# Optimization experiments

Hardware: AMD Instinct MI355X
Metric: run time of the kernel (lower is better)

Reference implementation:

```python
import jax, jax.numpy as jnp
import numpy as np

B, N, C = 2, 4096, 768
H = 12
D = C // H  # head_dim = 64
SCALE = D ** -0.5


def setup_inputs() -> dict:
    key = jax.random.key(0)
    ks = jax.random.split(key, 5)
    std = C ** -0.5
    return {
        "x": jax.random.normal(ks[0], (B, N, C), dtype=jnp.float32),
        "qkv_w": jax.random.normal(ks[1], (3 * C, C), dtype=jnp.float32) * std,
        "qkv_b": jnp.zeros((3 * C,), dtype=jnp.float32),
        "proj_w": jax.random.normal(ks[2], (C, C), dtype=jnp.float32) * std,
        "proj_b": jnp.zeros((C,), dtype=jnp.float32),
    }


def reference(x, qkv_w, qkv_b, proj_w, proj_b):
    b, n, c = x.shape
    # qkv projection: [B,N,3C] -> [3,B,H,N,D]
    qkv = (x @ qkv_w.T + qkv_b).reshape(b, n, 3, H, D).transpose(2, 0, 3, 1, 4)
    q, k, v = qkv[0], qkv[1], qkv[2]
    # scaled dot-product attention, explicit softmax (fused_attn=False path)
    attn = jnp.einsum("bhqd,bhkd->bhqk", q * SCALE, k)
    attn = jax.nn.softmax(attn, axis=-1)
    out = jnp.einsum("bhqk,bhkd->bhqd", attn, v)
    out = out.transpose(0, 2, 1, 3).reshape(b, n, c)
    return out @ proj_w.T + proj_b
```

## Files before the change

kernel.cpp:

```cpp
#include <hip/hip_runtime.h>
#include <hip/hip_bf16.h>
#include <stdint.h>

#define DEV __device__ __forceinline__

typedef __bf16 bf16_t;
typedef bf16_t bf16x8 __attribute__((ext_vector_type(8)));
typedef float f32x4 __attribute__((ext_vector_type(4)));
typedef unsigned long long ull;

union Frag { bf16x8 v; ull h[2]; };

struct __align__(16) Pack16 { ull lo, hi; };

DEV unsigned short f2b(float f) {
  bf16_t b = (bf16_t)f;
  return __builtin_bit_cast(unsigned short, b);
}

DEV void async_copy16(void* lds, const void* gsrc) {
  __builtin_amdgcn_global_load_lds(
      (const __attribute__((address_space(1))) unsigned int*)(uintptr_t)gsrc,
      (__attribute__((address_space(3))) unsigned int*)(uintptr_t)lds,
      16, 0, 0);
}

#define MFMA16x16x32(a, b, c) __builtin_amdgcn_mfma_f32_16x16x32_bf16((a), (b), (c), 0, 0, 0)

#define QSCALE 0.18033688011112042f

__global__ __launch_bounds__(256) void k_cvt_all(
    const float* __restrict__ s0, Pack16* __restrict__ d0, int n0,
    const float* __restrict__ s1, Pack16* __restrict__ d1, int n1,
    const float* __restrict__ s2, Pack16* __restrict__ d2, int n2) {
  int i = blockIdx.x * 256 + threadIdx.x;
  const float* src; Pack16* dst; int idx;
  if (i < n0) { src = s0; dst = d0; idx = i; }
  else if (i < n0 + n1) { src = s1; dst = d1; idx = i - n0; }
  else if (i < n0 + n1 + n2) { src = s2; dst = d2; idx = i - n0 - n1; }
  else return;
  const float4* s4 = (const float4*)src + 2 * (size_t)idx;
  float4 a = s4[0], b = s4[1];
  union { unsigned short u[8]; Pack16 p; } P;
  P.u[0] = f2b(a.x); P.u[1] = f2b(a.y); P.u[2] = f2b(a.z); P.u[3] = f2b(a.w);
  P.u[4] = f2b(b.x); P.u[5] = f2b(b.y); P.u[6] = f2b(b.z); P.u[7] = f2b(b.w);
  dst[idx] = P.p;
}

template <int EPI>
__global__ __launch_bounds__(256) void k_gemm(
    const unsigned short* __restrict__ A, const unsigned short* __restrict__ Bw,
    const float* __restrict__ bias,
    unsigned short* __restrict__ qp, unsigned short* __restrict__ kp,
    unsigned short* __restrict__ vtp, float* __restrict__ outp,
    int Nn, int K, int nt_n) {
  __shared__ char LDS[2 * 32768];
  const int tid = threadIdx.x;
  const int lane = tid & 63, wid = tid >> 6;
  const int g = lane >> 4, lq = lane & 15;
  const int tm = blockIdx.x / nt_n, tn = blockIdx.x % nt_n;
  const int m0 = tm * 128, n0 = tn * 128;
  const int wm = (wid >> 1) * 64, wn = (wid & 1) * 64;
  const size_t rowbytes = (size_t)K * 2;
  const int nk = K >> 6;
  f32x4 acc[4][4] = {};

  const char* aga[4];
  const char* bga[4];
#pragma unroll
  for (int pass = 0; pass < 4; ++pass) {
    int c = pass * 256 + tid;
    int r = c >> 3;
    int cb = ((c & 7) * 16) ^ ((r & 7) << 4);
    aga[pass] = (const char*)A + (size_t)(m0 + r) * rowbytes + cb;
    bga[pass] = (const char*)Bw + (size_t)(n0 + r) * rowbytes + cb;
  }

#pragma unroll
  for (int pass = 0; pass < 4; ++pass) {
    async_copy16(LDS + pass * 4096 + tid * 16, aga[pass]);
    async_copy16(LDS + 16384 + pass * 4096 + tid * 16, bga[pass]);
    aga[pass] += 128; bga[pass] += 128;
  }
  asm volatile("s_waitcnt vmcnt(0)" ::: "memory");
  __syncthreads();

  int buf = 0;
  for (int ks = 0; ks < nk; ++ks) {
    if (ks < nk - 1) {
      char* nb = LDS + (buf ^ 1) * 32768;
#pragma unroll
      for (int pass = 0; pass < 4; ++pass) {
        async_copy16(nb + pass * 4096 + tid * 16, aga[pass]);
        async_copy16(nb + 16384 + pass * 4096 + tid * 16, bga[pass]);
        aga[pass] += 128; bga[pass] += 128;
      }
    }
    const char* Ab = LDS + buf * 32768;
    const char* Bb = Ab + 16384;
#pragma unroll
    for (int kk = 0; kk < 2; ++kk) {
      Frag aF[4], bF[4];
#pragma unroll
      for (int f = 0; f < 4; ++f) {
        int ra = wm + f * 16 + lq;
        aF[f].v = *(const bf16x8*)(Ab + ra * 128 +
                                   ((kk * 64 + 16 * g) ^ ((ra & 7) << 4)));
        int rb = wn + f * 16 + lq;
        bF[f].v = *(const bf16x8*)(Bb + rb * 128 +
                                   ((kk * 64 + 16 * g) ^ ((rb & 7) << 4)));
      }
#pragma unroll
      for (int fm = 0; fm < 4; ++fm)
#pragma unroll
        for (int fn = 0; fn < 4; ++fn)
          acc[fm][fn] = MFMA16x16x32(aF[fm].v, bF[fn].v, acc[fm][fn]);
    }
    asm volatile("s_waitcnt vmcnt(0)" ::: "memory");
    __syncthreads();
    buf ^= 1;
  }

  if (EPI == 0) {
    const int which = tm / 6;
    const float sc = (which == 0) ? QSCALE : 1.0f;
#pragma unroll
    for (int fm = 0; fm < 4; ++fm) {
#pragma unroll
      for (int fn = 0; fn < 4; ++fn) {
        int f = m0 + wm + fm * 16 + 4 * g;
        int t = n0 + wn + fn * 16 + lq;
        int rem = f - which * 768;
        int hh = rem >> 6, ddb = rem & 63;
        int bb = t >> 12, tr = t & 4095;
        int bh = bb * 12 + hh;
        float4 bq = *(const float4*)(bias + f);
        float bvr[4] = {bq.x, bq.y, bq.z, bq.w};
        if (which == 2) {
#pragma unroll
          for (int r = 0; r < 4; ++r) {
            int d = ddb + r;
            size_t off = (size_t)bh * 262144 + (size_t)(tr >> 6) * 4096 +
                         (size_t)((d >> 4) * 2 + ((tr >> 5) & 1)) * 512 +
                         (size_t)(((tr >> 2) & 3) * 16 + (d & 15)) * 8 +
                         (size_t)((tr >> 4) & 1) * 4 + (size_t)(tr & 3);
            vtp[off] = f2b(acc[fm][fn][r] + bvr[r]);
          }
        } else {
          unsigned short* dst = (which == 0) ? qp : kp;
          union { unsigned short u[4]; ull q; } pk;
#pragma unroll
          for (int r = 0; r < 4; ++r) pk.u[r] = f2b((acc[fm][fn][r] + bvr[r]) * sc);
          *(ull*)(dst + ((size_t)bh * 4096 + tr) * 64 + ddb) = pk.q;
        }
      }
    }
  } else {
#pragma unroll
    for (int fm = 0; fm < 4; ++fm)
#pragma unroll
      for (int fn = 0; fn < 4; ++fn) {
        int f = m0 + wm + fm * 16 + 4 * g;
        int t = n0 + wn + fn * 16 + lq;
        float4 bq = *(const float4*)(bias + f);
        float4 o4;
        o4.x = acc[fm][fn][0] + bq.x;
        o4.y = acc[fm][fn][1] + bq.y;
        o4.z = acc[fm][fn][2] + bq.z;
        o4.w = acc[fm][fn][3] + bq.w;
        *(float4*)(outp + (size_t)t * Nn + f) = o4;
      }
  }
}

__global__ __launch_bounds__(256) void k_attn(
    const unsigned short* __restrict__ qp, const unsigned short* __restrict__ kp,
    const unsigned short* __restrict__ vtp, unsigned short* __restrict__ ao) {
  __shared__ unsigned short KsA[2 * 4096];
  __shared__ unsigned short VsA[2 * 4096];
  const int tid = threadIdx.x;
  const int lane = tid & 63, wid = tid >> 6;
  const int g = lane >> 4, lq = lane & 15;
  const int bh = blockIdx.x % 24, qb = blockIdx.x / 24;
  const int q0 = qb * 128 + wid * 16;
  const unsigned short* qbase = qp + ((size_t)bh * 4096 + q0) * 64;

  Frag qF[2][2];
#pragma unroll
  for (int grp = 0; grp < 2; ++grp)
#pragma unroll
    for (int kk = 0; kk < 2; ++kk)
      qF[grp][kk].v = *(const bf16x8*)(qbase + grp * 4096 + lq * 64 + kk * 32 + 8 * g);

  const char* kga0; const char* kga1;
  const char* vga0; const char* vga1;
  {
    int c = tid;
    int krow = (c >> 7) * 16 + (c & 15);
    int kbyte = ((c >> 6) & 1) * 64 + ((c >> 4) & 3) * 16;
    kga0 = (const char*)(kp + (size_t)bh * 262144) + (size_t)krow * 128 + kbyte;
    kga1 = kga0 + 4096;
    vga0 = (const char*)(vtp + (size_t)bh * 262144) + (size_t)c * 16;
    vga1 = vga0 + 4096;
  }
  char* ldsK = (char*)KsA + tid * 16;
  char* ldsV = (char*)VsA + tid * 16;

  Frag oneF;
#pragma unroll
  for (int j = 0; j < 8; ++j) oneF.v[j] = (bf16_t)1.0f;

  f32x4 o[2][4] = {};
  f32x4 l_acc[2] = {};

  async_copy16(ldsK, kga0);
  async_copy16(ldsK + 4096, kga1);
  async_copy16(ldsV, vga0);
  async_copy16(ldsV + 4096, vga1);
  kga0 += 8192; kga1 += 8192; vga0 += 8192; vga1 += 8192;
  asm volatile("s_waitcnt vmcnt(0)" ::: "memory");
  __syncthreads();

  int cur = 0;
  for (int t = 0; t < 64; ++t) {
    if (t < 63) {
      int nb = (cur ^ 1) * 8192;
      async_copy16(ldsK + nb, kga0);
      async_copy16(ldsK + nb + 4096, kga1);
      async_copy16(ldsV + nb, vga0);
      async_copy16(ldsV + nb + 4096, vga1);
      kga0 += 8192; kga1 += 8192; vga0 += 8192; vga1 += 8192;
    }
    const char* Kb = (const char*)KsA + cur * 8192 + lane * 16;
    const char* Vb = (const char*)VsA + cur * 8192 + lane * 16;

    f32x4 s0[4], s1[4];
    __builtin_amdgcn_s_setprio(1);
#pragma unroll
    for (int fn = 0; fn < 4; ++fn) {
      Frag k0F, k1F;
      k0F.v = *(const bf16x8*)(Kb + (fn * 2 + 0) * 1024);
      k1F.v = *(const bf16x8*)(Kb + (fn * 2 + 1) * 1024);
      f32x4 a0 = {0.f, 0.f, 0.f, 0.f}, a1 = {0.f, 0.f, 0.f, 0.f};
      a0 = MFMA16x16x32(k0F.v, qF[0][0].v, a0);
      a0 = MFMA16x16x32(k1F.v, qF[0][1].v, a0);
      a1 = MFMA16x16x32(k0F.v, qF[1][0].v, a1);
      a1 = MFMA16x16x32(k1F.v, qF[1][1].v, a1);
      s0[fn] = a0; s1[fn] = a1;
    }
    __builtin_amdgcn_s_setprio(0);

    Frag pA0[2], pA1[2];
#pragma unroll
    for (int kk = 0; kk < 2; ++kk)
#pragma unroll
      for (int j = 0; j < 4; ++j) {
        pA0[kk].v[j]     = (bf16_t)__builtin_amdgcn_exp2f(s0[2 * kk][j]);
        pA0[kk].v[4 + j] = (bf16_t)__builtin_amdgcn_exp2f(s0[2 * kk + 1][j]);
        pA1[kk].v[j]     = (bf16_t)__builtin_amdgcn_exp2f(s1[2 * kk][j]);
        pA1[kk].v[4 + j] = (bf16_t)__builtin_amdgcn_exp2f(s1[2 * kk + 1][j]);
      }

    __builtin_amdgcn_s_setprio(1);
    l_acc[0] = MFMA16x16x32(oneF.v, pA0[0].v, l_acc[0]);
    l_acc[0] = MFMA16x16x32(oneF.v, pA0[1].v, l_acc[0]);
    l_acc[1] = MFMA16x16x32(oneF.v, pA1[0].v, l_acc[1]);
    l_acc[1] = MFMA16x16x32(oneF.v, pA1[1].v, l_acc[1]);
#pragma unroll
    for (int d = 0; d < 4; ++d) {
      Frag v0F, v1F;
      v0F.v = *(const bf16x8*)(Vb + (d * 2 + 0) * 1024);
      v1F.v = *(const bf16x8*)(Vb + (d * 2 + 1) * 1024);
      o[0][d] = MFMA16x16x32(v0F.v, pA0[0].v, o[0][d]);
      o[0][d] = MFMA16x16x32(v1F.v, pA0[1].v, o[0][d]);
      o[1][d] = MFMA16x16x32(v0F.v, pA1[0].v, o[1][d]);
      o[1][d] = MFMA16x16x32(v1F.v, pA1[1].v, o[1][d]);
    }
    __builtin_amdgcn_s_setprio(0);

    asm volatile("s_waitcnt vmcnt(0)" ::: "memory");
    __syncthreads();
    cur ^= 1;
  }

  const int bb = bh / 12, hh = bh % 12;
#pragma unroll
  for (int grp = 0; grp < 2; ++grp) {
    float rl = __builtin_amdgcn_rcpf(l_acc[grp][0]);
    int q = q0 + grp * 64 + lq;
    unsigned short* dst = ao + ((size_t)(bb * 4096 + q)) * 768 + hh * 64;
#pragma unroll
    for (int d = 0; d < 4; ++d) {
      union { unsigned short u[4]; ull qw; } pk;
#pragma unroll
      for (int r = 0; r < 4; ++r) pk.u[r] = f2b(o[grp][d][r] * rl);
      *(ull*)(dst + d * 16 + 4 * g) = pk.qw;
    }
  }
}

extern "C" void kernel_launch(void* const* d_in, const int* in_sizes, int n_in,
                              void* d_out, int out_size, void* d_ws, size_t ws_size,
                              hipStream_t stream) {
  (void)in_sizes; (void)n_in; (void)out_size; (void)ws_size;
  const float* x = (const float*)d_in[0];
  const float* qkv_w = (const float*)d_in[1];
  const float* qkv_b = (const float*)d_in[2];
  const float* proj_w = (const float*)d_in[3];
  const float* proj_b = (const float*)d_in[4];
  float* out = (float*)d_out;
  unsigned short* ws = (unsigned short*)d_ws;

  unsigned short* xb    = ws;
  unsigned short* wqkv  = ws + 6291456;
  unsigned short* wproj = ws + 8060928;
  unsigned short* qp    = ws + 8650752;
  unsigned short* kp    = ws + 14942208;
  unsigned short* vtp   = ws + 21233664;
  unsigned short* ao    = xb;

  k_cvt_all<<<4224, 256, 0, stream>>>(x, (Pack16*)xb, 786432,
                                      qkv_w, (Pack16*)wqkv, 221184,
                                      proj_w, (Pack16*)wproj, 73728);

  k_gemm<0><<<18 * 64, 256, 0, stream>>>(wqkv, xb, qkv_b, qp, kp, vtp, nullptr,
                                         2304, 768, 64);
  k_attn<<<768, 256, 0, stream>>>(qp, kp, vtp, ao);
  k_gemm<1><<<6 * 64, 256, 0, stream>>>(wproj, ao, proj_b, nullptr, nullptr, nullptr,
                                        out, 768, 768, 64);
}
```

Baseline: 269.3 us.

## Prefetch two tiles ahead with partial vmcnt waits in GEMM and attention loops

Both the GEMM and the attention kernels now issue async global-to-LDS loads two stages ahead instead of one. Each iteration waits only for the older stage (partial vmcnt), reads the whole tile from LDS into registers, then barriers and refills that same buffer while the MFMAs run. This removes the full vmcnt(0) drain and end-of-iteration syncthreads that serialized memory and compute. The cost is more live registers for the preloaded fragments, which may lower occupancy, and an extra barrier per iteration.

Measured after the change: 291.9 us. +8.4%, slower.

```diff
diff --git a/kernel.cpp b/kernel.cpp
--- a/kernel.cpp
+++ b/kernel.cpp
@@ -76,49 +76,54 @@
     bga[pass] = (const char*)Bw + (size_t)(n0 + r) * rowbytes + cb;
   }
 
-#pragma unroll
-  for (int pass = 0; pass < 4; ++pass) {
-    async_copy16(LDS + pass * 4096 + tid * 16, aga[pass]);
-    async_copy16(LDS + 16384 + pass * 4096 + tid * 16, bga[pass]);
-    aga[pass] += 128; bga[pass] += 128;
-  }
-  asm volatile("s_waitcnt vmcnt(0)" ::: "memory");
-  __syncthreads();
-
-  int buf = 0;
+  auto stageAB = [&](int bufoff) {
+#pragma unroll
+    for (int pass = 0; pass < 4; ++pass) {
+      async_copy16(LDS + bufoff + pass * 4096 + tid * 16, aga[pass]);
+      async_copy16(LDS + bufoff + 16384 + pass * 4096 + tid * 16, bga[pass]);
+      aga[pass] += 128; bga[pass] += 128;
+    }
+  };
+
+  stageAB(0);
+  stageAB(32768);
+
   for (int ks = 0; ks < nk; ++ks) {
-    if (ks < nk - 1) {
-      char* nb = LDS + (buf ^ 1) * 32768;
-#pragma unroll
-      for (int pass = 0; pass < 4; ++pass) {
-        async_copy16(nb + pass * 4096 + tid * 16, aga[pass]);
-        async_copy16(nb + 16384 + pass * 4096 + tid * 16, bga[pass]);
-        aga[pass] += 128; bga[pass] += 128;
-      }
-    }
-    const char* Ab = LDS + buf * 32768;
+    if (ks < nk - 1)
+      asm volatile("s_waitcnt vmcnt(8)" ::: "memory");
+    else
+      asm volatile("s_waitcnt vmcnt(0)" ::: "memory");
+    __builtin_amdgcn_s_barrier();
+
+    const char* Ab = LDS + (ks & 1) * 32768;
     const char* Bb = Ab + 16384;
-#pragma unroll
-    for (int kk = 0; kk < 2; ++kk) {
-      Frag aF[4], bF[4];
+    Frag aF[2][4], bF[2][4];
+#pragma unroll
+    for (int kk = 0; kk < 2; ++kk)
 #pragma unroll
       for (int f = 0; f < 4; ++f) {
         int ra = wm + f * 16 + lq;
-        aF[f].v = *(const bf16x8*)(Ab + ra * 128 +
-                                   ((kk * 64 + 16 * g) ^ ((ra & 7) << 4)));
+        aF[kk][f].v = *(const bf16x8*)(Ab + ra * 128 +
+                                       ((kk * 64 + 16 * g) ^ ((ra & 7) << 4)));
         int rb = wn + f * 16 + lq;
-        bF[f].v = *(const bf16x8*)(Bb + rb * 128 +
-                                   ((kk * 64 + 16 * g) ^ ((rb & 7) << 4)));
+        bF[kk][f].v = *(const bf16x8*)(Bb + rb * 128 +
+                                       ((kk * 64 + 16 * g) ^ ((rb & 7) << 4)));
       }
+    asm volatile("s_waitcnt lgkmcnt(0)" ::: "memory");
+    __builtin_amdgcn_sched_barrier(0);
+    __builtin_amdgcn_s_barrier();
+
+    if (ks + 2 < nk) stageAB((ks & 1) * 32768);
+
+    __builtin_amdgcn_s_setprio(1);
+#pragma unroll
+    for (int kk = 0; kk < 2; ++kk)
 #pragma unroll
       for (int fm = 0; fm < 4; ++fm)
 #pragma unroll
         for (int fn = 0; fn < 4; ++fn)
-          acc[fm][fn] = MFMA16x16x32(aF[fm].v, bF[fn].v, acc[fm][fn]);
-    }
-    asm volatile("s_waitcnt vmcnt(0)" ::: "memory");
-    __syncthreads();
-    buf ^= 1;
+          acc[fm][fn] = MFMA16x16x32(aF[kk][fm].v, bF[kk][fn].v, acc[fm][fn]);
+    __builtin_amdgcn_s_setprio(0);
   }
 
   if (EPI == 0) {
@@ -206,6 +211,14 @@
   char* ldsK = (char*)KsA + tid * 16;
   char* ldsV = (char*)VsA + tid * 16;
 
+  auto stageKV = [&](int bufoff) {
+    async_copy16(ldsK + bufoff, kga0);
+    async_copy16(ldsK + bufoff + 4096, kga1);
+    async_copy16(ldsV + bufoff, vga0);
+    async_copy16(ldsV + bufoff + 4096, vga1);
+    kga0 += 8192; kga1 += 8192; vga0 += 8192; vga1 += 8192;
+  };
+
   Frag oneF;
 #pragma unroll
   for (int j = 0; j < 8; ++j) oneF.v[j] = (bf16_t)1.0f;
@@ -213,39 +226,40 @@
   f32x4 o[2][4] = {};
   f32x4 l_acc[2] = {};
 
-  async_copy16(ldsK, kga0);
-  async_copy16(ldsK + 4096, kga1);
-  async_copy16(ldsV, vga0);
-  async_copy16(ldsV + 4096, vga1);
-  kga0 += 8192; kga1 += 8192; vga0 += 8192; vga1 += 8192;
-  asm volatile("s_waitcnt vmcnt(0)" ::: "memory");
-  __syncthreads();
-
-  int cur = 0;
+  stageKV(0);
+  stageKV(8192);
+
   for (int t = 0; t < 64; ++t) {
-    if (t < 63) {
-      int nb = (cur ^ 1) * 8192;
-      async_copy16(ldsK + nb, kga0);
-      async_copy16(ldsK + nb + 4096, kga1);
-      async_copy16(ldsV + nb, vga0);
-      async_copy16(ldsV + nb + 4096, vga1);
-      kga0 += 8192; kga1 += 8192; vga0 += 8192; vga1 += 8192;
-    }
-    const char* Kb = (const char*)KsA + cur * 8192 + lane * 16;
-    const char* Vb = (const char*)VsA + cur * 8192 + lane * 16;
+    if (t < 63)
+      asm volatile("s_waitcnt vmcnt(4)" ::: "memory");
+    else
+      asm volatile("s_waitcnt vmcnt(0)" ::: "memory");
+    __builtin_amdgcn_s_barrier();
+
+    const int cb = (t & 1) * 8192;
+    const char* Kb = (const char*)KsA + cb + lane * 16;
+    const char* Vb = (const char*)VsA + cb + lane * 16;
+    Frag kF[8], vF[8];
+#pragma unroll
+    for (int i = 0; i < 8; ++i) {
+      kF[i].v = *(const bf16x8*)(Kb + i * 1024);
+      vF[i].v = *(const bf16x8*)(Vb + i * 1024);
+    }
+    asm volatile("s_waitcnt lgkmcnt(0)" ::: "memory");
+    __builtin_amdgcn_sched_barrier(0);
+    __builtin_amdgcn_s_barrier();
+
+    if (t < 62) stageKV(cb);
 
     f32x4 s0[4], s1[4];
     __builtin_amdgcn_s_setprio(1);
 #pragma unroll
     for (int fn = 0; fn < 4; ++fn) {
-      Frag k0F, k1F;
-      k0F.v = *(const bf16x8*)(Kb + (fn * 2 + 0) * 1024);
-      k1F.v = *(const bf16x8*)(Kb + (fn * 2 + 1) * 1024);
       f32x4 a0 = {0.f, 0.f, 0.f, 0.f}, a1 = {0.f, 0.f, 0.f, 0.f};
-      a0 = MFMA16x16x32(k0F.v, qF[0][0].v, a0);
-      a0 = MFMA16x16x32(k1F.v, qF[0][1].v, a0);
-      a1 = MFMA16x16x32(k0F.v, qF[1][0].v, a1);
-      a1 = MFMA16x16x32(k1F.v, qF[1][1].v, a1);
+      a0 = MFMA16x16x32(kF[2 * fn].v, qF[0][0].v, a0);
+      a0 = MFMA16x16x32(kF[2 * fn + 1].v, qF[0][1].v, a0);
+      a1 = MFMA16x16x32(kF[2 * fn].v, qF[1][0].v, a1);
+      a1 = MFMA16x16x32(kF[2 * fn + 1].v, qF[1][1].v, a1);
       s0[fn] = a0; s1[fn] = a1;
     }
     __builtin_amdgcn_s_setprio(0);
@@ -268,19 +282,12 @@
     l_acc[1] = MFMA16x16x32(oneF.v, pA1[1].v, l_acc[1]);
 #pragma unroll
     for (int d = 0; d < 4; ++d) {
-      Frag v0F, v1F;
-      v0F.v = *(const bf16x8*)(Vb + (d * 2 + 0) * 1024);
-      v1F.v = *(const bf16x8*)(Vb + (d * 2 + 1) * 1024);
-      o[0][d] = MFMA16x16x32(v0F.v, pA0[0].v, o[0][d]);
-      o[0][d] = MFMA16x16x32(v1F.v, pA0[1].v, o[0][d]);
-      o[1][d] = MFMA16x16x32(v0F.v, pA1[0].v, o[1][d]);
-      o[1][d] = MFMA16x16x32(v1F.v, pA1[1].v, o[1][d]);
+      o[0][d] = MFMA16x16x32(vF[2 * d].v, pA0[0].v, o[0][d]);
+      o[0][d] = MFMA16x16x32(vF[2 * d + 1].v, pA0[1].v, o[0][d]);
+      o[1][d] = MFMA16x16x32(vF[2 * d].v, pA1[0].v, o[1][d]);
+      o[1][d] = MFMA16x16x32(vF[2 * d + 1].v, pA1[1].v, o[1][d]);
     }
     __builtin_amdgcn_s_setprio(0);
-
-    asm volatile("s_waitcnt vmcnt(0)" ::: "memory");
-    __syncthreads();
-    cur ^= 1;
   }
 
   const int bb = bh / 12, hh = bh % 12;
```

## Triple-buffer GEMM and attention loads with one barrier per step and 512-thread GEMM

Applied to the files above, without the earlier changes.

Both the GEMM and attention kernels move from double to triple-buffered LDS staging. Each iteration waits with a partial vmcnt and a single barrier, then issues the prefetch two tiles ahead, replacing the full drain at the end of every step. The GEMM also grows to 512 threads (8 waves, each computing a 64x32 sub-tile) and raises MFMA priority. Per-block LDS rises, which may cut occupancy, and each wave in the GEMM gets less register reuse.

New measurement: 277.5 us. +3.1%, slower.

```diff
diff --git a/kernel.cpp b/kernel.cpp
--- a/kernel.cpp
+++ b/kernel.cpp
@@ -48,64 +48,75 @@
 }
 
 template <int EPI>
-__global__ __launch_bounds__(256) void k_gemm(
+__global__ __launch_bounds__(512) void k_gemm(
     const unsigned short* __restrict__ A, const unsigned short* __restrict__ Bw,
     const float* __restrict__ bias,
     unsigned short* __restrict__ qp, unsigned short* __restrict__ kp,
     unsigned short* __restrict__ vtp, float* __restrict__ outp,
     int Nn, int K, int nt_n) {
-  __shared__ char LDS[2 * 32768];
+  __shared__ char LDS[3 * 32768];
   const int tid = threadIdx.x;
   const int lane = tid & 63, wid = tid >> 6;
   const int g = lane >> 4, lq = lane & 15;
   const int tm = blockIdx.x / nt_n, tn = blockIdx.x % nt_n;
   const int m0 = tm * 128, n0 = tn * 128;
-  const int wm = (wid >> 1) * 64, wn = (wid & 1) * 64;
+  const int wm = (wid >> 2) * 64, wn = (wid & 3) * 32;
   const size_t rowbytes = (size_t)K * 2;
   const int nk = K >> 6;
-  f32x4 acc[4][4] = {};
-
-  const char* aga[4];
-  const char* bga[4];
-#pragma unroll
-  for (int pass = 0; pass < 4; ++pass) {
-    int c = pass * 256 + tid;
+  f32x4 acc[4][2] = {};
+
+  const char* aga[2];
+  const char* bga[2];
+#pragma unroll
+  for (int pass = 0; pass < 2; ++pass) {
+    int c = pass * 512 + tid;
     int r = c >> 3;
     int cb = ((c & 7) * 16) ^ ((r & 7) << 4);
     aga[pass] = (const char*)A + (size_t)(m0 + r) * rowbytes + cb;
     bga[pass] = (const char*)Bw + (size_t)(n0 + r) * rowbytes + cb;
   }
 
-#pragma unroll
-  for (int pass = 0; pass < 4; ++pass) {
-    async_copy16(LDS + pass * 4096 + tid * 16, aga[pass]);
-    async_copy16(LDS + 16384 + pass * 4096 + tid * 16, bga[pass]);
-    aga[pass] += 128; bga[pass] += 128;
-  }
-  asm volatile("s_waitcnt vmcnt(0)" ::: "memory");
-  __syncthreads();
-
-  int buf = 0;
+  auto stageAB = [&](int bufoff) {
+#pragma unroll
+    for (int pass = 0; pass < 2; ++pass) {
+      async_copy16(LDS + bufoff + pass * 8192 + tid * 16, aga[pass]);
+      async_copy16(LDS + bufoff + 16384 + pass * 8192 + tid * 16, bga[pass]);
+      aga[pass] += 128; bga[pass] += 128;
+    }
+  };
+
+  stageAB(0);
+  stageAB(32768);
+
+  int rbuf = 0, sbuf = 2;
   for (int ks = 0; ks < nk; ++ks) {
-    if (ks < nk - 1) {
-      char* nb = LDS + (buf ^ 1) * 32768;
-#pragma unroll
-      for (int pass = 0; pass < 4; ++pass) {
-        async_copy16(nb + pass * 4096 + tid * 16, aga[pass]);
-        async_copy16(nb + 16384 + pass * 4096 + tid * 16, bga[pass]);
-        aga[pass] += 128; bga[pass] += 128;
-      }
-    }
-    const char* Ab = LDS + buf * 32768;
+    if (ks < nk - 1)
+      asm volatile("s_waitcnt vmcnt(4)" ::: "memory");
+    else
+      asm volatile("s_waitcnt vmcnt(0)" ::: "memory");
+    __builtin_amdgcn_s_barrier();
+
+    if (ks + 2 < nk) {
+      stageAB(sbuf * 32768);
+      sbuf = (sbuf == 2) ? 0 : sbuf + 1;
+    }
+
+    const char* Ab = LDS + rbuf * 32768;
     const char* Bb = Ab + 16384;
+    rbuf = (rbuf == 2) ? 0 : rbuf + 1;
+
+    __builtin_amdgcn_s_setprio(1);
 #pragma unroll
     for (int kk = 0; kk < 2; ++kk) {
-      Frag aF[4], bF[4];
+      Frag aF[4], bF[2];
 #pragma unroll
       for (int f = 0; f < 4; ++f) {
         int ra = wm + f * 16 + lq;
         aF[f].v = *(const bf16x8*)(Ab + ra * 128 +
                                    ((kk * 64 + 16 * g) ^ ((ra & 7) << 4)));
+      }
+#pragma unroll
+      for (int f = 0; f < 2; ++f) {
         int rb = wn + f * 16 + lq;
         bF[f].v = *(const bf16x8*)(Bb + rb * 128 +
                                    ((kk * 64 + 16 * g) ^ ((rb & 7) << 4)));
@@ -113,12 +124,10 @@
 #pragma unroll
       for (int fm = 0; fm < 4; ++fm)
 #pragma unroll
-        for (int fn = 0; fn < 4; ++fn)
+        for (int fn = 0; fn < 2; ++fn)
           acc[fm][fn] = MFMA16x16x32(aF[fm].v, bF[fn].v, acc[fm][fn]);
     }
-    asm volatile("s_waitcnt vmcnt(0)" ::: "memory");
-    __syncthreads();
-    buf ^= 1;
+    __builtin_amdgcn_s_setprio(0);
   }
 
   if (EPI == 0) {
@@ -127,7 +136,7 @@
 #pragma unroll
     for (int fm = 0; fm < 4; ++fm) {
 #pragma unroll
-      for (int fn = 0; fn < 4; ++fn) {
+      for (int fn = 0; fn < 2; ++fn) {
         int f = m0 + wm + fm * 16 + 4 * g;
         int t = n0 + wn + fn * 16 + lq;
         int rem = f - which * 768;
@@ -159,7 +168,7 @@
 #pragma unroll
     for (int fm = 0; fm < 4; ++fm)
 #pragma unroll
-      for (int fn = 0; fn < 4; ++fn) {
+      for (int fn = 0; fn < 2; ++fn) {
         int f = m0 + wm + fm * 16 + 4 * g;
         int t = n0 + wn + fn * 16 + lq;
         float4 bq = *(const float4*)(bias + f);
@@ -176,8 +185,8 @@
 __global__ __launch_bounds__(256) void k_attn(
     const unsigned short* __restrict__ qp, const unsigned short* __restrict__ kp,
     const unsigned short* __restrict__ vtp, unsigned short* __restrict__ ao) {
-  __shared__ unsigned short KsA[2 * 4096];
-  __shared__ unsigned short VsA[2 * 4096];
+  __shared__ unsigned short KsA[3 * 4096];
+  __shared__ unsigned short VsA[3 * 4096];
   const int tid = threadIdx.x;
   const int lane = tid & 63, wid = tid >> 6;
   const int g = lane >> 4, lq = lane & 15;
@@ -206,6 +215,14 @@
   char* ldsK = (char*)KsA + tid * 16;
   char* ldsV = (char*)VsA + tid * 16;
 
+  auto stageKV = [&](int bufoff) {
+    async_copy16(ldsK + bufoff, kga0);
+    async_copy16(ldsK + bufoff + 4096, kga1);
+    async_copy16(ldsV + bufoff, vga0);
+    async_copy16(ldsV + bufoff + 4096, vga1);
+    kga0 += 8192; kga1 += 8192; vga0 += 8192; vga1 += 8192;
+  };
+
   Frag oneF;
 #pragma unroll
   for (int j = 0; j < 8; ++j) oneF.v[j] = (bf16_t)1.0f;
@@ -213,26 +230,25 @@
   f32x4 o[2][4] = {};
   f32x4 l_acc[2] = {};
 
-  async_copy16(ldsK, kga0);
-  async_copy16(ldsK + 4096, kga1);
-  async_copy16(ldsV, vga0);
-  async_copy16(ldsV + 4096, vga1);
-  kga0 += 8192; kga1 += 8192; vga0 += 8192; vga1 += 8192;
-  asm volatile("s_waitcnt vmcnt(0)" ::: "memory");
-  __syncthreads();
-
-  int cur = 0;
+  stageKV(0);
+  stageKV(8192);
+
+  int rbuf = 0, sbuf = 2;
   for (int t = 0; t < 64; ++t) {
-    if (t < 63) {
-      int nb = (cur ^ 1) * 8192;
-      async_copy16(ldsK + nb, kga0);
-      async_copy16(ldsK + nb + 4096, kga1);
-      async_copy16(ldsV + nb, vga0);
-      async_copy16(ldsV + nb + 4096, vga1);
-      kga0 += 8192; kga1 += 8192; vga0 += 8192; vga1 += 8192;
-    }
-    const char* Kb = (const char*)KsA + cur * 8192 + lane * 16;
-    const char* Vb = (const char*)VsA + cur * 8192 + lane * 16;
+    if (t < 63)
+      asm volatile("s_waitcnt vmcnt(4)" ::: "memory");
+    else
+      asm volatile("s_waitcnt vmcnt(0)" ::: "memory");
+    __builtin_amdgcn_s_barrier();
+
+    if (t < 62) {
+      stageKV(sbuf * 8192);
+      sbuf = (sbuf == 2) ? 0 : sbuf + 1;
+    }
+
+    const char* Kb = (const char*)KsA + rbuf * 8192 + lane * 16;
+    const char* Vb = (const char*)VsA + rbuf * 8192 + lane * 16;
+    rbuf = (rbuf == 2) ? 0 : rbuf + 1;
 
     f32x4 s0[4], s1[4];
     __builtin_amdgcn_s_setprio(1);
@@ -277,10 +293,6 @@
       o[1][d] = MFMA16x16x32(v1F.v, pA1[1].v, o[1][d]);
     }
     __builtin_amdgcn_s_setprio(0);
-
-    asm volatile("s_waitcnt vmcnt(0)" ::: "memory");
-    __syncthreads();
-    cur ^= 1;
   }
 
   const int bb = bh / 12, hh = bh % 12;
@@ -323,9 +335,9 @@
                                       qkv_w, (Pack16*)wqkv, 221184,
                                       proj_w, (Pack16*)wproj, 73728);
 
-  k_gemm<0><<<18 * 64, 256, 0, stream>>>(wqkv, xb, qkv_b, qp, kp, vtp, nullptr,
+  k_gemm<0><<<18 * 64, 512, 0, stream>>>(wqkv, xb, qkv_b, qp, kp, vtp, nullptr,
                                          2304, 768, 64);
   k_attn<<<768, 256, 0, stream>>>(qp, kp, vtp, ao);
-  k_gemm<1><<<6 * 64, 256, 0, stream>>>(wproj, ao, proj_b, nullptr, nullptr, nullptr,
+  k_gemm<1><<<6 * 64, 512, 0, stream>>>(wproj, ao, proj_b, nullptr, nullptr, nullptr,
                                         out, 768, 768, 64);
 }
```
